# Kernel optimization log

Measured on AMD Instinct MI355X. Metric: run time of the kernel, lower is better.

## Reference

```python
import jax, jax.numpy as jnp
import numpy as np

N0, N1, N2 = 100000, 20000, 4000
DEG = 10
G_NODES = 200000
D, ED, CD, FF, NHEAD = 512, 256, 300, 2048, 2


def _layernorm(x, g, b, eps=1e-5):
    m = jnp.mean(x, -1, keepdims=True)
    v = jnp.var(x, -1, keepdims=True)
    return (x - m) * jax.lax.rsqrt(v + eps) * g + b


def _mha(q_in, kv_in, w_in, b_in, w_out, b_out):
    # torch nn.MultiheadAttention, inputs are (seq, batch, d)
    d = q_in.shape[-1]
    wq, wk, wv = w_in[:d], w_in[d:2 * d], w_in[2 * d:]
    bq, bk, bv = b_in[:d], b_in[d:2 * d], b_in[2 * d:]
    dh = d // NHEAD
    q = (q_in @ wq.T + bq).reshape(q_in.shape[0], q_in.shape[1], NHEAD, dh)
    k = (kv_in @ wk.T + bk).reshape(kv_in.shape[0], kv_in.shape[1], NHEAD, dh)
    v = (kv_in @ wv.T + bv).reshape(kv_in.shape[0], kv_in.shape[1], NHEAD, dh)
    scores = jnp.einsum('qnhd,knhd->nhqk', q, k) * (dh ** -0.5)
    o = jnp.einsum('nhqk,knhd->qnhd', jax.nn.softmax(scores, -1), v)
    o = o.reshape(q_in.shape[0], q_in.shape[1], d)
    return o @ w_out.T + b_out


def setup_inputs() -> dict:
    key = jax.random.key(0)
    k = lambda i: jax.random.fold_in(key, i)
    inp = {}
    inp['nid0'] = jax.random.randint(k(0), (N0,), 0, G_NODES, dtype=jnp.int32)
    inp['nid1'] = jax.random.randint(k(1), (N1,), 0, G_NODES, dtype=jnp.int32)
    inp['nid2'] = jax.random.randint(k(2), (N2,), 0, G_NODES, dtype=jnp.int32)
    inp['esrc0'] = jax.random.randint(k(3), (N1 * DEG,), 0, N0, dtype=jnp.int32)
    inp['edst0'] = jnp.repeat(jnp.arange(N1, dtype=jnp.int32), DEG)
    inp['esrc1'] = jax.random.randint(k(4), (N2 * DEG,), 0, N1, dtype=jnp.int32)
    inp['edst1'] = jnp.repeat(jnp.arange(N2, dtype=jnp.int32), DEG)
    inp['content0'] = jax.random.normal(k(5), (N0, CD), jnp.float32)
    inp['content1'] = jax.random.normal(k(6), (N1, CD), jnp.float32)
    inp['content2'] = jax.random.normal(k(7), (N2, CD), jnp.float32)
    inp['node_emb_w'] = jax.random.normal(k(8), (G_NODES + 1, ED), jnp.float32) / ED
    inp['ee_w'] = jax.random.normal(k(9), (D, ED), jnp.float32) * 0.06
    inp['ee_b'] = jax.random.normal(k(10), (D,), jnp.float32) * 0.001
    inp['proj_w'] = jax.random.normal(k(11), (D, CD), jnp.float32) * 0.06
    inp['proj_b'] = jax.random.normal(k(12), (D,), jnp.float32) * 0.001
    inp['proj_g'] = jnp.ones((D,), jnp.float32)
    inp['proj_beta'] = jnp.zeros((D,), jnp.float32)
    L = 2  # decoder layers
    inp['sa_in_w'] = jax.random.normal(k(13), (L, 3 * D, D), jnp.float32) * 0.04
    inp['sa_in_b'] = jnp.zeros((L, 3 * D), jnp.float32)
    inp['sa_out_w'] = jax.random.normal(k(14), (L, D, D), jnp.float32) * 0.04
    inp['sa_out_b'] = jnp.zeros((L, D), jnp.float32)
    inp['ca_in_w'] = jax.random.normal(k(15), (L, 3 * D, D), jnp.float32) * 0.04
    inp['ca_in_b'] = jnp.zeros((L, 3 * D), jnp.float32)
    inp['ca_out_w'] = jax.random.normal(k(16), (L, D, D), jnp.float32) * 0.04
    inp['ca_out_b'] = jnp.zeros((L, D), jnp.float32)
    inp['lin1_w'] = jax.random.normal(k(17), (L, FF, D), jnp.float32) * 0.03
    inp['lin1_b'] = jnp.zeros((L, FF), jnp.float32)
    inp['lin2_w'] = jax.random.normal(k(18), (L, D, FF), jnp.float32) * 0.03
    inp['lin2_b'] = jnp.zeros((L, D), jnp.float32)
    for n in ('n1', 'n2', 'n3'):
        inp[n + '_g'] = jnp.ones((L, D), jnp.float32)
        inp[n + '_b'] = jnp.zeros((L, D), jnp.float32)
    return inp


def _forward(nid0, nid1, nid2, esrc0, edst0, esrc1, edst1,
             content0, content1, content2, node_emb_w, ee_w, ee_b,
             proj_w, proj_b, proj_g, proj_beta,
             sa_in_w, sa_in_b, sa_out_w, sa_out_b,
             ca_in_w, ca_in_b, ca_out_w, ca_out_b,
             lin1_w, lin1_b, lin2_w, lin2_b,
             n1_g, n1_b, n2_g, n2_b, n3_g, n3_b):
    def node_h(nid, content):
        nh = node_emb_w[nid + 1] @ ee_w.T + ee_b           # emb_expand(node_emb(nid+1))
        c = _layernorm(jax.nn.leaky_relu(content @ proj_w.T + proj_b, 0.1), proj_g, proj_beta)
        h = nh + c                                          # mix_embeddings (c[:, :D] == c)
        return h / jnp.maximum(jnp.linalg.norm(h, axis=1, keepdims=True), 1e-5)

    h0 = node_h(nid0, content0)
    h1 = node_h(nid1, content1)
    h2 = node_h(nid2, content2)

    def agg_mean(h_src, src, dst, n_dst):
        s = jax.ops.segment_sum(h_src[src], dst, num_segments=n_dst)
        w = jax.ops.segment_sum(jnp.ones(src.shape[0], h_src.dtype), dst, num_segments=n_dst)
        return s / w[:, None]

    # block 0: non-prediction GraphConv -> concat(mean_agg, h), L2 normalize
    m1 = agg_mean(h0, esrc0, edst0, N1)
    h1 = jnp.concatenate([m1, h1], axis=1)                  # (N1, 2D)
    h1 = h1 / jnp.maximum(jnp.linalg.norm(h1, axis=1, keepdims=True), 1e-5)

    # block 1: prediction GraphConv -> transformer-decoder fusion
    m2 = agg_mean(h1, esrc1, edst1, N2)                     # (N2, 2D)
    mem = m2.reshape(N2, 2, D).transpose(1, 0, 2)           # (n_layer=2, N2, D)
    tgt = h2[None]                                          # (1, N2, D)
    for l in range(2):  # post-norm TransformerDecoderLayer, gelu, dropout=0
        t2 = _mha(tgt, tgt, sa_in_w[l], sa_in_b[l], sa_out_w[l], sa_out_b[l])
        tgt = _layernorm(tgt + t2, n1_g[l], n1_b[l])
        t2 = _mha(tgt, mem, ca_in_w[l], ca_in_b[l], ca_out_w[l], ca_out_b[l])
        tgt = _layernorm(tgt + t2, n2_g[l], n2_b[l])
        ff = jax.nn.gelu(tgt @ lin1_w[l].T + lin1_b[l], approximate=False) @ lin2_w[l].T + lin2_b[l]
        tgt = _layernorm(tgt + ff, n3_g[l], n3_b[l])
    out = tgt[0]                                            # squeeze -> (N2, D)
    return out / jnp.maximum(jnp.linalg.norm(out, axis=1, keepdims=True), 1e-5)


def reference(nid0, nid1, nid2, esrc0, edst0, esrc1, edst1,
              content0, content1, content2, node_emb_w, ee_w, ee_b,
              proj_w, proj_b, proj_g, proj_beta,
              sa_in_w, sa_in_b, sa_out_w, sa_out_b,
              ca_in_w, ca_in_b, ca_out_w, ca_out_b,
              lin1_w, lin1_b, lin2_w, lin2_b,
              n1_g, n1_b, n2_g, n2_b, n3_g, n3_b):
    return _forward(nid0, nid1, nid2, esrc0, edst0, esrc1, edst1,
                    content0, content1, content2, node_emb_w, ee_w, ee_b,
                    proj_w, proj_b, proj_g, proj_beta,
                    sa_in_w, sa_in_b, sa_out_w, sa_out_b,
                    ca_in_w, ca_in_b, ca_out_w, ca_out_b,
                    lin1_w, lin1_b, lin2_w, lin2_b,
                    n1_g, n1_b, n2_g, n2_b, n3_g, n3_b)
```

## Files before the change

kernel.cpp:

```cpp
#include <hip/hip_runtime.h>
#include <math.h>

static constexpr int kN0  = 100000;
static constexpr int kN1  = 20000;
static constexpr int kN2  = 4000;
static constexpr int kDeg = 10;
static constexpr int kD   = 512;
static constexpr int kFF  = 2048;
static constexpr int kRows  = 48;
static constexpr int kRowsN = 32;
static constexpr int kLdA  = 584;
static constexpr int kLdG  = 520;

using short8  = __attribute__((ext_vector_type(8))) short;
using floatx4 = __attribute__((ext_vector_type(4))) float;

__device__ inline unsigned short f2bf(float f) {
    union { float f; unsigned u; } v; v.f = f;
    unsigned r = v.u + 0x7FFFu + ((v.u >> 16) & 1u);
    return (unsigned short)(r >> 16);
}

__global__ __launch_bounds__(256) void pack_node_w_kernel(
    const float* __restrict__ ee_w, const float* __restrict__ proj_w,
    ushort* __restrict__ Bp)
{
    int tid  = blockIdx.x * 256 + threadIdx.x;
    int lane = tid & 63;
    int tile = tid >> 6;
    int n     = (tile & 31) * 16 + (lane & 15);
    int kbase = (tile >> 5) * 32 + (lane >> 4) * 8;
    ushort v[8];
    #pragma unroll
    for (int j = 0; j < 8; ++j) {
        int k = kbase + j;
        float f = 0.f;
        if (k < 256)      f = ee_w[(size_t)n * 256 + k];
        else if (k < 556) f = proj_w[(size_t)n * 300 + (k - 256)];
        v[j] = f2bf(f);
    }
    uint4 u;
    u.x = (unsigned)v[0] | ((unsigned)v[1] << 16);
    u.y = (unsigned)v[2] | ((unsigned)v[3] << 16);
    u.z = (unsigned)v[4] | ((unsigned)v[5] << 16);
    u.w = (unsigned)v[6] | ((unsigned)v[7] << 16);
    *(uint4*)(Bp + (size_t)tid * 8) = u;
}

__global__ __launch_bounds__(256) void pack512_many_kernel(
    const float* __restrict__ sa_in_w, const float* __restrict__ sa_out_w,
    const float* __restrict__ ca_in_w, const float* __restrict__ ca_out_w,
    ushort* __restrict__ dst)
{
    int y = blockIdx.y, l = y / 6, m = y % 6;
    const float* W;
    switch (m) {
        case 0: W = sa_in_w  + (size_t)l * 3 * kD * kD + (size_t)2 * kD * kD; break;
        case 1: W = sa_out_w + (size_t)l * kD * kD; break;
        case 2: W = ca_in_w  + (size_t)l * 3 * kD * kD; break;
        case 3: W = ca_in_w  + (size_t)l * 3 * kD * kD + (size_t)kD * kD; break;
        case 4: W = ca_in_w  + (size_t)l * 3 * kD * kD + (size_t)2 * kD * kD; break;
        default:W = ca_out_w + (size_t)l * kD * kD; break;
    }
    int tid  = blockIdx.x * 256 + threadIdx.x;
    int lane = tid & 63;
    int tile = tid >> 6;
    int n  = (tile & 31) * 16 + (lane & 15);
    int kb = (tile >> 5) * 32 + (lane >> 4) * 8;
    const float* src = W + (size_t)n * 512 + kb;
    ushort v[8];
    #pragma unroll
    for (int j = 0; j < 8; ++j) v[j] = f2bf(src[j]);
    uint4 u;
    u.x = (unsigned)v[0] | ((unsigned)v[1] << 16);
    u.y = (unsigned)v[2] | ((unsigned)v[3] << 16);
    u.z = (unsigned)v[4] | ((unsigned)v[5] << 16);
    u.w = (unsigned)v[6] | ((unsigned)v[7] << 16);
    *(uint4*)(dst + (size_t)y * 262144 + (size_t)tid * 8) = u;
}

__global__ __launch_bounds__(256) void pack_generic_kernel(
    const float* __restrict__ src, size_t srcStride,
    ushort* __restrict__ dst, size_t dstStride, int N, int K)
{
    int tid  = blockIdx.x * 256 + threadIdx.x;
    int NT = N >> 4;
    int lane = tid & 63;
    int tile = tid >> 6;
    int ct = tile % NT, kc = tile / NT;
    int n  = ct * 16 + (lane & 15);
    int kb = kc * 32 + (lane >> 4) * 8;
    const float* W = src + blockIdx.y * srcStride + (size_t)n * K + kb;
    ushort v[8];
    #pragma unroll
    for (int j = 0; j < 8; ++j) v[j] = f2bf(W[j]);
    uint4 u;
    u.x = (unsigned)v[0] | ((unsigned)v[1] << 16);
    u.y = (unsigned)v[2] | ((unsigned)v[3] << 16);
    u.z = (unsigned)v[4] | ((unsigned)v[5] << 16);
    u.w = (unsigned)v[6] | ((unsigned)v[7] << 16);
    *(uint4*)(dst + blockIdx.y * dstStride + (size_t)tid * 8) = u;
}

__global__ __launch_bounds__(512, 4) void node_h_mfma(
    const int* __restrict__ nid,
    const float* __restrict__ content,
    const float* __restrict__ node_emb_w,
    const ushort* __restrict__ Bp,
    const float* __restrict__ ee_b, const float* __restrict__ proj_b,
    const float* __restrict__ proj_g, const float* __restrict__ proj_beta,
    float* __restrict__ hout, int ldh, int n)
{
    __shared__ __align__(16) ushort As[kRowsN * kLdA];
    __shared__ float redS[8][kRowsN], redQ[8][kRowsN];
    __shared__ float meanv[kRowsN], rstdv[kRowsN], rowinv[kRowsN];

    const int t    = threadIdx.x;
    const int lane = t & 63;
    const int wv   = t >> 6;
    const int quad = lane >> 4;
    const int l15  = lane & 15;
    const int row0 = blockIdx.x * kRowsN;

    #pragma unroll
    for (int it = 0; it < 9; ++it) {
        int flat = it * 512 + t;
        int r  = flat / 144;
        int k4 = flat - r * 144;
        int row = row0 + r; if (row >= n) row = n - 1;
        float4 f = make_float4(0.f, 0.f, 0.f, 0.f);
        if (k4 < 64)
            f = *(const float4*)(node_emb_w + ((size_t)(nid[row] + 1)) * 256 + k4 * 4);
        else if (k4 < 139)
            f = *(const float4*)(content + (size_t)row * 300 + (k4 - 64) * 4);
        ushort4 o = make_ushort4(f2bf(f.x), f2bf(f.y), f2bf(f.z), f2bf(f.w));
        *(ushort4*)(As + (size_t)r * kLdA + k4 * 4) = o;
    }
    __syncthreads();

    floatx4 acc[2][4] = {};
    const short8* BpV = (const short8*)Bp;

    #pragma unroll
    for (int kc = 8; kc < 18; ++kc) {
        const short8* bp = BpV + (size_t)(kc * 32 + wv * 4) * 64 + lane;
        short8 b0 = bp[0], b1 = bp[64], b2 = bp[128], b3 = bp[192];
        short8 a[2];
        #pragma unroll
        for (int rt = 0; rt < 2; ++rt)
            a[rt] = *(const short8*)(As + (size_t)(rt * 16 + l15) * kLdA + kc * 32 + quad * 8);
        #pragma unroll
        for (int rt = 0; rt < 2; ++rt) {
            acc[rt][0] = __builtin_amdgcn_mfma_f32_16x16x32_bf16(a[rt], b0, acc[rt][0], 0, 0, 0);
            acc[rt][1] = __builtin_amdgcn_mfma_f32_16x16x32_bf16(a[rt], b1, acc[rt][1], 0, 0, 0);
            acc[rt][2] = __builtin_amdgcn_mfma_f32_16x16x32_bf16(a[rt], b2, acc[rt][2], 0, 0, 0);
            acc[rt][3] = __builtin_amdgcn_mfma_f32_16x16x32_bf16(a[rt], b3, acc[rt][3], 0, 0, 0);
        }
    }

    const int colbase = wv * 64 + l15;
    float pb[4], pg[4], pbt[4], eb[4];
    #pragma unroll
    for (int ct = 0; ct < 4; ++ct) {
        int c = colbase + ct * 16;
        pb[ct]  = proj_b[c];
        pg[ct]  = proj_g[c];
        pbt[ct] = proj_beta[c];
        eb[ct]  = ee_b[c];
    }

    float s8[8], q8[8];
    #pragma unroll
    for (int rt = 0; rt < 2; ++rt) {
        #pragma unroll
        for (int i = 0; i < 4; ++i) {
            float s = 0.f, q = 0.f;
            #pragma unroll
            for (int ct = 0; ct < 4; ++ct) {
                float c = acc[rt][ct][i] + pb[ct];
                c = (c >= 0.f) ? c : 0.1f * c;
                acc[rt][ct][i] = c;
                s += c; q = fmaf(c, c, q);
            }
            s8[rt * 4 + i] = s; q8[rt * 4 + i] = q;
        }
    }
    #pragma unroll
    for (int idx = 0; idx < 8; ++idx) {
        #pragma unroll
        for (int m = 1; m < 16; m <<= 1) {
            s8[idx] += __shfl_xor(s8[idx], m);
            q8[idx] += __shfl_xor(q8[idx], m);
        }
    }
    if (l15 == 0) {
        #pragma unroll
        for (int rt = 0; rt < 2; ++rt)
            #pragma unroll
            for (int i = 0; i < 4; ++i) {
                int rl = rt * 16 + quad * 4 + i;
                redS[wv][rl] = s8[rt * 4 + i];
                redQ[wv][rl] = q8[rt * 4 + i];
            }
    }
    __syncthreads();
    if (t < kRowsN) {
        float s = 0.f, q = 0.f;
        #pragma unroll
        for (int w = 0; w < 8; ++w) { s += redS[w][t]; q += redQ[w][t]; }
        float m   = s * (1.f / 512.f);
        float var = q * (1.f / 512.f) - m * m;
        meanv[t] = m;
        rstdv[t] = rsqrtf(var + 1e-5f);
    }
    __syncthreads();

    #pragma unroll
    for (int rt = 0; rt < 2; ++rt) {
        #pragma unroll
        for (int i = 0; i < 4; ++i) {
            int rl = rt * 16 + quad * 4 + i;
            float m = meanv[rl], rs = rstdv[rl];
            #pragma unroll
            for (int ct = 0; ct < 4; ++ct)
                acc[rt][ct][i] = (acc[rt][ct][i] - m) * rs * pg[ct] + pbt[ct] + eb[ct];
        }
    }

    #pragma unroll
    for (int kc = 0; kc < 8; ++kc) {
        const short8* bp = BpV + (size_t)(kc * 32 + wv * 4) * 64 + lane;
        short8 b0 = bp[0], b1 = bp[64], b2 = bp[128], b3 = bp[192];
        short8 a[2];
        #pragma unroll
        for (int rt = 0; rt < 2; ++rt)
            a[rt] = *(const short8*)(As + (size_t)(rt * 16 + l15) * kLdA + kc * 32 + quad * 8);
        #pragma unroll
        for (int rt = 0; rt < 2; ++rt) {
            acc[rt][0] = __builtin_amdgcn_mfma_f32_16x16x32_bf16(a[rt], b0, acc[rt][0], 0, 0, 0);
            acc[rt][1] = __builtin_amdgcn_mfma_f32_16x16x32_bf16(a[rt], b1, acc[rt][1], 0, 0, 0);
            acc[rt][2] = __builtin_amdgcn_mfma_f32_16x16x32_bf16(a[rt], b2, acc[rt][2], 0, 0, 0);
            acc[rt][3] = __builtin_amdgcn_mfma_f32_16x16x32_bf16(a[rt], b3, acc[rt][3], 0, 0, 0);
        }
    }

    #pragma unroll
    for (int rt = 0; rt < 2; ++rt) {
        #pragma unroll
        for (int i = 0; i < 4; ++i) {
            float psq = 0.f;
            #pragma unroll
            for (int ct = 0; ct < 4; ++ct)
                psq = fmaf(acc[rt][ct][i], acc[rt][ct][i], psq);
            q8[rt * 4 + i] = psq;
        }
    }
    #pragma unroll
    for (int idx = 0; idx < 8; ++idx)
        #pragma unroll
        for (int m = 1; m < 16; m <<= 1)
            q8[idx] += __shfl_xor(q8[idx], m);
    if (l15 == 0) {
        #pragma unroll
        for (int rt = 0; rt < 2; ++rt)
            #pragma unroll
            for (int i = 0; i < 4; ++i)
                redS[wv][rt * 16 + quad * 4 + i] = q8[rt * 4 + i];
    }
    __syncthreads();
    if (t < kRowsN) {
        float s = 0.f;
        #pragma unroll
        for (int w = 0; w < 8; ++w) s += redS[w][t];
        rowinv[t] = 1.f / fmaxf(sqrtf(s), 1e-5f);
    }
    __syncthreads();

    #pragma unroll
    for (int rt = 0; rt < 2; ++rt) {
        #pragma unroll
        for (int i = 0; i < 4; ++i) {
            int rl = rt * 16 + quad * 4 + i;
            int grow = row0 + rl;
            if (grow < n) {
                float inv = rowinv[rl];
                float* dst = hout + (size_t)grow * ldh + colbase;
                #pragma unroll
                for (int ct = 0; ct < 4; ++ct)
                    dst[ct * 16] = acc[rt][ct][i] * inv;
            }
        }
    }
}

__device__ inline float gelu_exact(float x) {
    return 0.5f * x * (1.f + erff(x * 0.70710678118654752f));
}

template<int EPI>
__global__ __launch_bounds__(512, 2) void gemm_mfma(
    const float* __restrict__ A, int lda,
    const ushort* __restrict__ Bp, const float* __restrict__ bias,
    float* __restrict__ C, int ldc,
    const float* __restrict__ resid,
    const float* __restrict__ lng, const float* __restrict__ lnb,
    int M, int K, int N)
{
    __shared__ __align__(16) ushort As[kRows * kLdG];
    __shared__ float redS[8][kRows], redQ[8][kRows];
    __shared__ float meanv[kRows], rstdv[kRows];

    const int t    = threadIdx.x;
    const int lane = t & 63;
    const int wv   = t >> 6;
    const int quad = lane >> 4;
    const int l15  = lane & 15;
    const int row0 = blockIdx.x * kRows;
    const int nb   = blockIdx.y;
    const int NT   = N >> 4;

    floatx4 acc[3][4] = {};
    const short8* BpV = (const short8*)Bp;

    for (int k0 = 0; k0 < K; k0 += 512) {
        #pragma unroll
        for (int it = 0; it < 12; ++it) {
            int flat = it * 512 + t;
            int r  = flat >> 7;
            int k4 = flat & 127;
            int row = row0 + r; if (row >= M) row = M - 1;
            float4 f = *(const float4*)(A + (size_t)row * lda + k0 + k4 * 4);
            ushort4 o = make_ushort4(f2bf(f.x), f2bf(f.y), f2bf(f.z), f2bf(f.w));
            *(ushort4*)(As + (size_t)r * kLdG + k4 * 4) = o;
        }
        __syncthreads();
        const int g0 = k0 >> 5;
        #pragma unroll
        for (int kc = 0; kc < 16; ++kc) {
            const short8* bp = BpV + ((size_t)(g0 + kc) * NT + nb * 32 + wv * 4) * 64 + lane;
            short8 b0 = bp[0], b1 = bp[64], b2 = bp[128], b3 = bp[192];
            short8 a[3];
            #pragma unroll
            for (int rt = 0; rt < 3; ++rt)
                a[rt] = *(const short8*)(As + (size_t)(rt * 16 + l15) * kLdG + kc * 32 + quad * 8);
            #pragma unroll
            for (int rt = 0; rt < 3; ++rt) {
                acc[rt][0] = __builtin_amdgcn_mfma_f32_16x16x32_bf16(a[rt], b0, acc[rt][0], 0, 0, 0);
                acc[rt][1] = __builtin_amdgcn_mfma_f32_16x16x32_bf16(a[rt], b1, acc[rt][1], 0, 0, 0);
                acc[rt][2] = __builtin_amdgcn_mfma_f32_16x16x32_bf16(a[rt], b2, acc[rt][2], 0, 0, 0);
                acc[rt][3] = __builtin_amdgcn_mfma_f32_16x16x32_bf16(a[rt], b3, acc[rt][3], 0, 0, 0);
            }
        }
        __syncthreads();
    }

    const int colloc = wv * 64 + l15;
    float b[4];
    #pragma unroll
    for (int ct = 0; ct < 4; ++ct) b[ct] = bias[nb * 512 + colloc + ct * 16];

    if constexpr (EPI == 0 || EPI == 1) {
        #pragma unroll
        for (int rt = 0; rt < 3; ++rt) {
            #pragma unroll
            for (int i = 0; i < 4; ++i) {
                int row = row0 + rt * 16 + quad * 4 + i;
                if (row < M) {
                    float* dst = C + (size_t)row * ldc + nb * 512 + colloc;
                    #pragma unroll
                    for (int ct = 0; ct < 4; ++ct) {
                        float v = acc[rt][ct][i] + b[ct];
                        if (EPI == 1) v = gelu_exact(v);
                        dst[ct * 16] = v;
                    }
                }
            }
        }
    } else {
        float lg[4], lb[4];
        #pragma unroll
        for (int ct = 0; ct < 4; ++ct) {
            lg[ct] = lng[colloc + ct * 16];
            lb[ct] = lnb[colloc + ct * 16];
        }
        float s12[12], q12[12];
        #pragma unroll
        for (int rt = 0; rt < 3; ++rt) {
            #pragma unroll
            for (int i = 0; i < 4; ++i) {
                int rl = rt * 16 + quad * 4 + i;
                int row = row0 + rl; if (row >= M) row = M - 1;
                const float* rr = resid + (size_t)row * 512 + colloc;
                float s = 0.f, q = 0.f;
                #pragma unroll
                for (int ct = 0; ct < 4; ++ct) {
                    float h = acc[rt][ct][i] + b[ct] + rr[ct * 16];
                    acc[rt][ct][i] = h;
                    s += h; q = fmaf(h, h, q);
                }
                s12[rt * 4 + i] = s; q12[rt * 4 + i] = q;
            }
        }
        #pragma unroll
        for (int idx = 0; idx < 12; ++idx) {
            #pragma unroll
            for (int m = 1; m < 16; m <<= 1) {
                s12[idx] += __shfl_xor(s12[idx], m);
                q12[idx] += __shfl_xor(q12[idx], m);
            }
        }
        if (l15 == 0) {
            #pragma unroll
            for (int rt = 0; rt < 3; ++rt)
                #pragma unroll
                for (int i = 0; i < 4; ++i) {
                    int rl = rt * 16 + quad * 4 + i;
                    redS[wv][rl] = s12[rt * 4 + i];
                    redQ[wv][rl] = q12[rt * 4 + i];
                }
        }
        __syncthreads();
        if (t < kRows) {
            float s = 0.f, q = 0.f;
            #pragma unroll
            for (int w = 0; w < 8; ++w) { s += redS[w][t]; q += redQ[w][t]; }
            float m   = s * (1.f / 512.f);
            float var = q * (1.f / 512.f) - m * m;
            meanv[t] = m;
            rstdv[t] = rsqrtf(var + 1e-5f);
        }
        __syncthreads();
        #pragma unroll
        for (int rt = 0; rt < 3; ++rt) {
            #pragma unroll
            for (int i = 0; i < 4; ++i) {
                int rl = rt * 16 + quad * 4 + i;
                int row = row0 + rl;
                if (row < M) {
                    float m = meanv[rl], rs = rstdv[rl];
                    float* dst = C + (size_t)row * 512 + colloc;
                    #pragma unroll
                    for (int ct = 0; ct < 4; ++ct)
                        dst[ct * 16] = (acc[rt][ct][i] - m) * rs * lg[ct] + lb[ct];
                }
            }
        }
    }
}

__global__ __launch_bounds__(512, 2) void gemm3_mfma(
    const float* __restrict__ A0, const ushort* __restrict__ B0,
    const float* __restrict__ b0p, float* __restrict__ C0, int M0,
    const float* __restrict__ A1, const ushort* __restrict__ B1,
    const float* __restrict__ b1p, float* __restrict__ C1, int M1,
    const float* __restrict__ A2, const ushort* __restrict__ B2,
    const float* __restrict__ b2p, float* __restrict__ C2, int M2)
{
    __shared__ __align__(16) ushort As[kRows * kLdG];

    const int t    = threadIdx.x;
    const int lane = t & 63;
    const int wv   = t >> 6;
    const int quad = lane >> 4;
    const int l15  = lane & 15;

    const int g0 = (M0 + kRows - 1) / kRows;
    const int g1 = (M1 + kRows - 1) / kRows;
    int bx = blockIdx.x;
    const float* A; const ushort* Bw; const float* bias; float* C; int M;
    if (bx < g0)           { A = A0; Bw = B0; bias = b0p; C = C0; M = M0; }
    else if (bx < g0 + g1) { bx -= g0; A = A1; Bw = B1; bias = b1p; C = C1; M = M1; }
    else                   { bx -= g0 + g1; A = A2; Bw = B2; bias = b2p; C = C2; M = M2; }
    const int row0 = bx * kRows;

    floatx4 acc[3][4] = {};
    const short8* BpV = (const short8*)Bw;

    #pragma unroll
    for (int it = 0; it < 12; ++it) {
        int flat = it * 512 + t;
        int r  = flat >> 7;
        int k4 = flat & 127;
        int row = row0 + r; if (row >= M) row = M - 1;
        float4 f = *(const float4*)(A + (size_t)row * 512 + k4 * 4);
        ushort4 o = make_ushort4(f2bf(f.x), f2bf(f.y), f2bf(f.z), f2bf(f.w));
        *(ushort4*)(As + (size_t)r * kLdG + k4 * 4) = o;
    }
    __syncthreads();
    #pragma unroll
    for (int kc = 0; kc < 16; ++kc) {
        const short8* bp = BpV + ((size_t)kc * 32 + wv * 4) * 64 + lane;
        short8 b0 = bp[0], b1 = bp[64], b2 = bp[128], b3 = bp[192];
        short8 a[3];
        #pragma unroll
        for (int rt = 0; rt < 3; ++rt)
            a[rt] = *(const short8*)(As + (size_t)(rt * 16 + l15) * kLdG + kc * 32 + quad * 8);
        #pragma unroll
        for (int rt = 0; rt < 3; ++rt) {
            acc[rt][0] = __builtin_amdgcn_mfma_f32_16x16x32_bf16(a[rt], b0, acc[rt][0], 0, 0, 0);
            acc[rt][1] = __builtin_amdgcn_mfma_f32_16x16x32_bf16(a[rt], b1, acc[rt][1], 0, 0, 0);
            acc[rt][2] = __builtin_amdgcn_mfma_f32_16x16x32_bf16(a[rt], b2, acc[rt][2], 0, 0, 0);
            acc[rt][3] = __builtin_amdgcn_mfma_f32_16x16x32_bf16(a[rt], b3, acc[rt][3], 0, 0, 0);
        }
    }

    const int colloc = wv * 64 + l15;
    float b[4];
    #pragma unroll
    for (int ct = 0; ct < 4; ++ct) b[ct] = bias[colloc + ct * 16];
    #pragma unroll
    for (int rt = 0; rt < 3; ++rt) {
        #pragma unroll
        for (int i = 0; i < 4; ++i) {
            int row = row0 + rt * 16 + quad * 4 + i;
            if (row < M) {
                float* dst = C + (size_t)row * 512 + colloc;
                #pragma unroll
                for (int ct = 0; ct < 4; ++ct)
                    dst[ct * 16] = acc[rt][ct][i] + b[ct];
            }
        }
    }
}

__device__ inline float block_sum256(float v, float* red4) {
    #pragma unroll
    for (int off = 32; off > 0; off >>= 1) v += __shfl_down(v, off);
    if ((threadIdx.x & 63) == 0) red4[threadIdx.x >> 6] = v;
    __syncthreads();
    return red4[0] + red4[1] + red4[2] + red4[3];
}

__global__ __launch_bounds__(256) void agg_norm1_kernel(
    const float* __restrict__ h0, const int* __restrict__ esrc,
    float* __restrict__ h1cat)
{
    __shared__ int idx[kDeg];
    __shared__ float red4[4];
    int i = blockIdx.x, t = threadIdx.x;
    if (t < kDeg) idx[t] = esrc[i * kDeg + t];
    __syncthreads();
    float s0 = 0.f, s1 = 0.f;
    for (int e = 0; e < kDeg; ++e) {
        const float* hr = h0 + (size_t)idx[e] * 512;
        s0 += hr[t]; s1 += hr[t + 256];
    }
    s0 *= 0.1f; s1 *= 0.1f;
    size_t base = (size_t)i * 1024;
    float o0 = h1cat[base + 512 + t];
    float o1 = h1cat[base + 768 + t];
    float tot = block_sum256(s0 * s0 + s1 * s1 + o0 * o0 + o1 * o1, red4);
    float inv = 1.f / fmaxf(sqrtf(tot), 1e-5f);
    h1cat[base + t]       = s0 * inv;
    h1cat[base + 256 + t] = s1 * inv;
    h1cat[base + 512 + t] = o0 * inv;
    h1cat[base + 768 + t] = o1 * inv;
}

__global__ __launch_bounds__(256) void agg2_kernel(
    const float* __restrict__ h1cat, const int* __restrict__ esrc,
    float* __restrict__ m2)
{
    __shared__ int idx[kDeg];
    int i = blockIdx.x, t = threadIdx.x;
    if (t < kDeg) idx[t] = esrc[i * kDeg + t];
    __syncthreads();
    float s0 = 0.f, s1 = 0.f, s2 = 0.f, s3 = 0.f;
    for (int e = 0; e < kDeg; ++e) {
        const float* hr = h1cat + (size_t)idx[e] * 1024;
        s0 += hr[t]; s1 += hr[t + 256]; s2 += hr[t + 512]; s3 += hr[t + 768];
    }
    size_t base = (size_t)i * 1024;
    m2[base + t]       = s0 * 0.1f;
    m2[base + 256 + t] = s1 * 0.1f;
    m2[base + 512 + t] = s2 * 0.1f;
    m2[base + 768 + t] = s3 * 0.1f;
}

__global__ __launch_bounds__(256) void attn_combine_kernel(
    const float* __restrict__ Q,
    const float* __restrict__ Kb, const float* __restrict__ Vb,
    float* __restrict__ O)
{
    __shared__ float red[4][4];
    __shared__ float a[4];
    int i = blockIdx.x, t = threadIdx.x;
    size_t base  = (size_t)i * 512;
    size_t base0 = (size_t)(2 * i) * 512;
    size_t base1 = base0 + 512;
    float q0 = Q[base + t], q1 = Q[base + t + 256];
    float p00 = q0 * Kb[base0 + t];
    float p01 = q0 * Kb[base1 + t];
    float p10 = q1 * Kb[base0 + t + 256];
    float p11 = q1 * Kb[base1 + t + 256];
    #pragma unroll
    for (int off = 32; off > 0; off >>= 1) {
        p00 += __shfl_down(p00, off);
        p01 += __shfl_down(p01, off);
        p10 += __shfl_down(p10, off);
        p11 += __shfl_down(p11, off);
    }
    int w = t >> 6;
    if ((t & 63) == 0) { red[w][0] = p00; red[w][1] = p01; red[w][2] = p10; red[w][3] = p11; }
    __syncthreads();
    if (t == 0) {
        float s00 = (red[0][0] + red[1][0] + red[2][0] + red[3][0]) * 0.0625f;
        float s01 = (red[0][1] + red[1][1] + red[2][1] + red[3][1]) * 0.0625f;
        float s10 = (red[0][2] + red[1][2] + red[2][2] + red[3][2]) * 0.0625f;
        float s11 = (red[0][3] + red[1][3] + red[2][3] + red[3][3]) * 0.0625f;
        float m0 = fmaxf(s00, s01);
        float e0 = expf(s00 - m0), e1 = expf(s01 - m0);
        float d0 = e0 + e1;
        a[0] = e0 / d0; a[1] = e1 / d0;
        float m1 = fmaxf(s10, s11);
        float f0 = expf(s10 - m1), f1 = expf(s11 - m1);
        float d1 = f0 + f1;
        a[2] = f0 / d1; a[3] = f1 / d1;
    }
    __syncthreads();
    O[base + t]       = a[0] * Vb[base0 + t]       + a[1] * Vb[base1 + t];
    O[base + t + 256] = a[2] * Vb[base0 + t + 256] + a[3] * Vb[base1 + t + 256];
}

__global__ __launch_bounds__(256) void final_norm_kernel(
    const float* __restrict__ tgt, float* __restrict__ out)
{
    __shared__ float red4[4];
    int i = blockIdx.x, t = threadIdx.x;
    size_t base = (size_t)i * 512;
    float v0 = tgt[base + t], v1 = tgt[base + t + 256];
    float tot = block_sum256(v0 * v0 + v1 * v1, red4);
    float inv = 1.f / fmaxf(sqrtf(tot), 1e-5f);
    out[base + t]       = v0 * inv;
    out[base + t + 256] = v1 * inv;
}

extern "C" void kernel_launch(void* const* d_in, const int* in_sizes, int n_in,
                              void* d_out, int out_size, void* d_ws, size_t ws_size,
                              hipStream_t stream)
{
    (void)in_sizes; (void)n_in; (void)out_size; (void)ws_size;
    const int*   nid0       = (const int*)d_in[0];
    const int*   nid1       = (const int*)d_in[1];
    const int*   nid2       = (const int*)d_in[2];
    const int*   esrc0      = (const int*)d_in[3];
    const int*   esrc1      = (const int*)d_in[5];
    const float* content0   = (const float*)d_in[7];
    const float* content1   = (const float*)d_in[8];
    const float* content2   = (const float*)d_in[9];
    const float* node_emb_w = (const float*)d_in[10];
    const float* ee_w       = (const float*)d_in[11];
    const float* ee_b       = (const float*)d_in[12];
    const float* proj_w     = (const float*)d_in[13];
    const float* proj_b     = (const float*)d_in[14];
    const float* proj_g     = (const float*)d_in[15];
    const float* proj_beta  = (const float*)d_in[16];
    const float* sa_in_w    = (const float*)d_in[17];
    const float* sa_in_b    = (const float*)d_in[18];
    const float* sa_out_w   = (const float*)d_in[19];
    const float* sa_out_b   = (const float*)d_in[20];
    const float* ca_in_w    = (const float*)d_in[21];
    const float* ca_in_b    = (const float*)d_in[22];
    const float* ca_out_w   = (const float*)d_in[23];
    const float* ca_out_b   = (const float*)d_in[24];
    const float* lin1_w     = (const float*)d_in[25];
    const float* lin1_b     = (const float*)d_in[26];
    const float* lin2_w     = (const float*)d_in[27];
    const float* lin2_b     = (const float*)d_in[28];
    const float* n1_g       = (const float*)d_in[29];
    const float* n1_b       = (const float*)d_in[30];
    const float* n2_g       = (const float*)d_in[31];
    const float* n2_b       = (const float*)d_in[32];
    const float* n3_g       = (const float*)d_in[33];
    const float* n3_b       = (const float*)d_in[34];

    float* ws = (float*)d_ws;
    size_t off = 0;
    float* h0    = ws + off; off += (size_t)kN0 * 512;
    float* h1cat = ws + off; off += (size_t)kN1 * 1024;
    float* m2    = ws + off; off += (size_t)kN2 * 1024;
    float* tgt   = ws + off; off += (size_t)kN2 * 512;
    float* Qb    = ws + off; off += (size_t)kN2 * 512;
    float* Kb    = ws + off; off += (size_t)2 * kN2 * 512;
    float* Vb    = ws + off; off += (size_t)2 * kN2 * 512;
    float* Ob    = ws + off; off += (size_t)kN2 * 512;
    float* ffh   = ws + off; off += (size_t)kN2 * 2048;
    ushort* BpNode = (ushort*)(ws + off); off += 147456;
    ushort* Pw512  = (ushort*)(ws + off); off += 12 * 262144 / 2;
    ushort* Pl1    = (ushort*)(ws + off); off += 2 * 1048576 / 2;
    ushort* Pl2    = (ushort*)(ws + off); off += 2 * 1048576 / 2;

    dim3 blk(256);

    pack_node_w_kernel<<<dim3(144), blk, 0, stream>>>(ee_w, proj_w, BpNode);
    pack512_many_kernel<<<dim3(128, 12), blk, 0, stream>>>(
        sa_in_w, sa_out_w, ca_in_w, ca_out_w, Pw512);
    pack_generic_kernel<<<dim3(512, 2), blk, 0, stream>>>(
        lin1_w, (size_t)kFF * kD, Pl1, 1048576, kFF, kD);
    pack_generic_kernel<<<dim3(512, 2), blk, 0, stream>>>(
        lin2_w, (size_t)kD * kFF, Pl2, 1048576, kD, kFF);

    node_h_mfma<<<dim3((kN0 + kRowsN - 1) / kRowsN), dim3(512), 0, stream>>>(
        nid0, content0, node_emb_w, BpNode, ee_b, proj_b, proj_g, proj_beta,
        h0, 512, kN0);
    node_h_mfma<<<dim3((kN1 + kRowsN - 1) / kRowsN), dim3(512), 0, stream>>>(
        nid1, content1, node_emb_w, BpNode, ee_b, proj_b, proj_g, proj_beta,
        h1cat + 512, 1024, kN1);
    node_h_mfma<<<dim3((kN2 + kRowsN - 1) / kRowsN), dim3(512), 0, stream>>>(
        nid2, content2, node_emb_w, BpNode, ee_b, proj_b, proj_g, proj_beta,
        tgt, 512, kN2);

    agg_norm1_kernel<<<dim3(kN1), blk, 0, stream>>>(h0, esrc0, h1cat);
    agg2_kernel<<<dim3(kN2), blk, 0, stream>>>(h1cat, esrc1, m2);

    const int M   = kN2;
    const int gM  = (M + kRows - 1) / kRows;
    const int gM2 = (2 * M + kRows - 1) / kRows;
    dim3 blk512(512);
    for (int l = 0; l < 2; ++l) {
        const ushort* sa_v_p   = Pw512 + (size_t)(l * 6 + 0) * 262144;
        const ushort* sa_out_p = Pw512 + (size_t)(l * 6 + 1) * 262144;
        const ushort* ca_q_p   = Pw512 + (size_t)(l * 6 + 2) * 262144;
        const ushort* ca_k_p   = Pw512 + (size_t)(l * 6 + 3) * 262144;
        const ushort* ca_v_p   = Pw512 + (size_t)(l * 6 + 4) * 262144;
        const ushort* ca_out_p = Pw512 + (size_t)(l * 6 + 5) * 262144;
        const ushort* l1_p     = Pl1 + (size_t)l * 1048576;
        const ushort* l2_p     = Pl2 + (size_t)l * 1048576;
        const float* sa_b = sa_in_b + (size_t)l * 3 * kD;
        const float* saob = sa_out_b + (size_t)l * kD;
        const float* ca_b = ca_in_b + (size_t)l * 3 * kD;
        const float* caob = ca_out_b + (size_t)l * kD;
        const float* l1b = lin1_b + (size_t)l * kFF;
        const float* l2b = lin2_b + (size_t)l * kD;

        gemm3_mfma<<<dim3(gM + gM2 + gM2), blk512, 0, stream>>>(
            tgt, sa_v_p, sa_b + 2 * kD, Qb, M,
            m2,  ca_k_p, ca_b + kD,     Kb, 2 * M,
            m2,  ca_v_p, ca_b + 2 * kD, Vb, 2 * M);

        gemm_mfma<2><<<dim3(gM, 1), blk512, 0, stream>>>(
            Qb, 512, sa_out_p, saob, tgt, 512,
            tgt, n1_g + l * kD, n1_b + l * kD, M, 512, 512);

        gemm_mfma<0><<<dim3(gM, 1), blk512, 0, stream>>>(
            tgt, 512, ca_q_p, ca_b, Qb, 512,
            nullptr, nullptr, nullptr, M, 512, 512);
        attn_combine_kernel<<<dim3(M), blk, 0, stream>>>(Qb, Kb, Vb, Ob);
        gemm_mfma<2><<<dim3(gM, 1), blk512, 0, stream>>>(
            Ob, 512, ca_out_p, caob, tgt, 512,
            tgt, n2_g + l * kD, n2_b + l * kD, M, 512, 512);

        gemm_mfma<1><<<dim3(gM, 4), blk512, 0, stream>>>(
            tgt, 512, l1_p, l1b, ffh, 2048,
            nullptr, nullptr, nullptr, M, 512, 2048);
        gemm_mfma<2><<<dim3(gM, 1), blk512, 0, stream>>>(
            ffh, 2048, l2_p, l2b, tgt, 512,
            tgt, n3_g + l * kD, n3_b + l * kD, M, 2048, 512);
    }

    final_norm_kernel<<<dim3(kN2), blk, 0, stream>>>(tgt, (float*)d_out);
}
```

Baseline: 1.112 ms.

## Store intermediate activations in bf16 and merge node-embedding launches

All intermediate activation buffers (h0, h1cat, m2, Q/K/V/O, ffh, and a bf16 copy of tgt) are now stored as bf16 instead of fp32. GEMMs load them directly without converting, and the gather/aggregate kernels widen bf16 to fp32 on read. This halves the memory traffic of the gather-heavy aggregation and of the GEMM A-operand loads. The three node_h launches are also merged into one grid. Storing aggregates and normalized vectors in bf16 adds extra rounding error before accumulation.

```diff
diff --git a/kernel.cpp b/kernel.cpp
--- a/kernel.cpp
+++ b/kernel.cpp
@@ -20,6 +20,9 @@
     unsigned r = v.u + 0x7FFFu + ((v.u >> 16) & 1u);
     return (unsigned short)(r >> 16);
 }
+__device__ inline float bf2f(ushort u) {
+    union { unsigned v; float f; } x; x.v = (unsigned)u << 16; return x.f;
+}
 
 __global__ __launch_bounds__(256) void pack_node_w_kernel(
     const float* __restrict__ ee_w, const float* __restrict__ proj_w,
@@ -103,13 +106,16 @@
 }
 
 __global__ __launch_bounds__(512, 4) void node_h_mfma(
-    const int* __restrict__ nid,
-    const float* __restrict__ content,
+    const int* __restrict__ nid0a, const float* __restrict__ content0a,
+    ushort* __restrict__ outB0, int n0,
+    const int* __restrict__ nid1a, const float* __restrict__ content1a,
+    ushort* __restrict__ outB1, int n1,
+    const int* __restrict__ nid2a, const float* __restrict__ content2a,
+    ushort* __restrict__ outB2, float* __restrict__ outF2, int n2,
     const float* __restrict__ node_emb_w,
     const ushort* __restrict__ Bp,
     const float* __restrict__ ee_b, const float* __restrict__ proj_b,
-    const float* __restrict__ proj_g, const float* __restrict__ proj_beta,
-    float* __restrict__ hout, int ldh, int n)
+    const float* __restrict__ proj_g, const float* __restrict__ proj_beta)
 {
     __shared__ __align__(16) ushort As[kRowsN * kLdA];
     __shared__ float redS[8][kRowsN], redQ[8][kRowsN];
@@ -120,7 +126,16 @@
     const int wv   = t >> 6;
     const int quad = lane >> 4;
     const int l15  = lane & 15;
-    const int row0 = blockIdx.x * kRowsN;
+
+    const int g0 = (n0 + kRowsN - 1) / kRowsN;
+    const int g1 = (n1 + kRowsN - 1) / kRowsN;
+    int bx = blockIdx.x;
+    const int* nid; const float* content; ushort* outB; float* outF = nullptr;
+    int ldh, n;
+    if (bx < g0)           { nid = nid0a; content = content0a; outB = outB0; ldh = 512;  n = n0; }
+    else if (bx < g0 + g1) { bx -= g0; nid = nid1a; content = content1a; outB = outB1; ldh = 1024; n = n1; }
+    else                   { bx -= g0 + g1; nid = nid2a; content = content2a; outB = outB2; outF = outF2; ldh = 512; n = n2; }
+    const int row0 = bx * kRowsN;
 
     #pragma unroll
     for (int it = 0; it < 9; ++it) {
@@ -284,10 +299,13 @@
             int grow = row0 + rl;
             if (grow < n) {
                 float inv = rowinv[rl];
-                float* dst = hout + (size_t)grow * ldh + colbase;
+                ushort* dB = outB + (size_t)grow * ldh + colbase;
                 #pragma unroll
-                for (int ct = 0; ct < 4; ++ct)
-                    dst[ct * 16] = acc[rt][ct][i] * inv;
+                for (int ct = 0; ct < 4; ++ct) {
+                    float v = acc[rt][ct][i] * inv;
+                    dB[ct * 16] = f2bf(v);
+                    if (outF) outF[(size_t)grow * ldh + colbase + ct * 16] = v;
+                }
             }
         }
     }
@@ -299,9 +317,9 @@
 
 template<int EPI>
 __global__ __launch_bounds__(512, 2) void gemm_mfma(
-    const float* __restrict__ A, int lda,
+    const ushort* __restrict__ A, int lda,
     const ushort* __restrict__ Bp, const float* __restrict__ bias,
-    float* __restrict__ C, int ldc,
+    ushort* __restrict__ Cb, float* __restrict__ Cf, int ldc,
     const float* __restrict__ resid,
     const float* __restrict__ lng, const float* __restrict__ lnb,
     int M, int K, int N)
@@ -324,14 +342,13 @@
 
     for (int k0 = 0; k0 < K; k0 += 512) {
         #pragma unroll
-        for (int it = 0; it < 12; ++it) {
+        for (int it = 0; it < 6; ++it) {
             int flat = it * 512 + t;
-            int r  = flat >> 7;
-            int k4 = flat & 127;
+            int r  = flat >> 6;
+            int k8 = flat & 63;
             int row = row0 + r; if (row >= M) row = M - 1;
-            float4 f = *(const float4*)(A + (size_t)row * lda + k0 + k4 * 4);
-            ushort4 o = make_ushort4(f2bf(f.x), f2bf(f.y), f2bf(f.z), f2bf(f.w));
-            *(ushort4*)(As + (size_t)r * kLdG + k4 * 4) = o;
+            short8 v = *(const short8*)(A + (size_t)row * lda + k0 + k8 * 8);
+            *(short8*)(As + (size_t)r * kLdG + k8 * 8) = v;
         }
         __syncthreads();
         const int g0 = k0 >> 5;
@@ -366,12 +383,12 @@
             for (int i = 0; i < 4; ++i) {
                 int row = row0 + rt * 16 + quad * 4 + i;
                 if (row < M) {
-                    float* dst = C + (size_t)row * ldc + nb * 512 + colloc;
+                    ushort* dst = Cb + (size_t)row * ldc + nb * 512 + colloc;
                     #pragma unroll
                     for (int ct = 0; ct < 4; ++ct) {
                         float v = acc[rt][ct][i] + b[ct];
                         if (EPI == 1) v = gelu_exact(v);
-                        dst[ct * 16] = v;
+                        dst[ct * 16] = f2bf(v);
                     }
                 }
             }
@@ -438,10 +455,14 @@
                 int row = row0 + rl;
                 if (row < M) {
                     float m = meanv[rl], rs = rstdv[rl];
-                    float* dst = C + (size_t)row * 512 + colloc;
+                    float*  dF = Cf + (size_t)row * 512 + colloc;
+                    ushort* dB = Cb + (size_t)row * 512 + colloc;
                     #pragma unroll
-                    for (int ct = 0; ct < 4; ++ct)
-                        dst[ct * 16] = (acc[rt][ct][i] - m) * rs * lg[ct] + lb[ct];
+                    for (int ct = 0; ct < 4; ++ct) {
+                        float v = (acc[rt][ct][i] - m) * rs * lg[ct] + lb[ct];
+                        dF[ct * 16] = v;
+                        dB[ct * 16] = f2bf(v);
+                    }
                 }
             }
         }
@@ -449,12 +470,12 @@
 }
 
 __global__ __launch_bounds__(512, 2) void gemm3_mfma(
-    const float* __restrict__ A0, const ushort* __restrict__ B0,
-    const float* __restrict__ b0p, float* __restrict__ C0, int M0,
-    const float* __restrict__ A1, const ushort* __restrict__ B1,
-    const float* __restrict__ b1p, float* __restrict__ C1, int M1,
-    const float* __restrict__ A2, const ushort* __restrict__ B2,
-    const float* __restrict__ b2p, float* __restrict__ C2, int M2)
+    const ushort* __restrict__ A0, const ushort* __restrict__ B0,
+    const float* __restrict__ b0p, ushort* __restrict__ C0, int M0,
+    const ushort* __restrict__ A1, const ushort* __restrict__ B1,
+    const float* __restrict__ b1p, ushort* __restrict__ C1, int M1,
+    const ushort* __restrict__ A2, const ushort* __restrict__ B2,
+    const float* __restrict__ b2p, ushort* __restrict__ C2, int M2)
 {
     __shared__ __align__(16) ushort As[kRows * kLdG];
 
@@ -467,7 +488,7 @@
     const int g0 = (M0 + kRows - 1) / kRows;
     const int g1 = (M1 + kRows - 1) / kRows;
     int bx = blockIdx.x;
-    const float* A; const ushort* Bw; const float* bias; float* C; int M;
+    const ushort* A; const ushort* Bw; const float* bias; ushort* C; int M;
     if (bx < g0)           { A = A0; Bw = B0; bias = b0p; C = C0; M = M0; }
     else if (bx < g0 + g1) { bx -= g0; A = A1; Bw = B1; bias = b1p; C = C1; M = M1; }
     else                   { bx -= g0 + g1; A = A2; Bw = B2; bias = b2p; C = C2; M = M2; }
@@ -477,14 +498,13 @@
     const short8* BpV = (const short8*)Bw;
 
     #pragma unroll
-    for (int it = 0; it < 12; ++it) {
+    for (int it = 0; it < 6; ++it) {
         int flat = it * 512 + t;
-        int r  = flat >> 7;
-        int k4 = flat & 127;
+        int r  = flat >> 6;
+        int k8 = flat & 63;
         int row = row0 + r; if (row >= M) row = M - 1;
-        float4 f = *(const float4*)(A + (size_t)row * 512 + k4 * 4);
-        ushort4 o = make_ushort4(f2bf(f.x), f2bf(f.y), f2bf(f.z), f2bf(f.w));
-        *(ushort4*)(As + (size_t)r * kLdG + k4 * 4) = o;
+        short8 v = *(const short8*)(A + (size_t)row * 512 + k8 * 8);
+        *(short8*)(As + (size_t)r * kLdG + k8 * 8) = v;
     }
     __syncthreads();
     #pragma unroll
@@ -514,10 +534,10 @@
         for (int i = 0; i < 4; ++i) {
             int row = row0 + rt * 16 + quad * 4 + i;
             if (row < M) {
-                float* dst = C + (size_t)row * 512 + colloc;
+                ushort* dst = C + (size_t)row * 512 + colloc;
                 #pragma unroll
                 for (int ct = 0; ct < 4; ++ct)
-                    dst[ct * 16] = acc[rt][ct][i] + b[ct];
+                    dst[ct * 16] = f2bf(acc[rt][ct][i] + b[ct]);
             }
         }
     }
@@ -532,8 +552,8 @@
 }
 
 __global__ __launch_bounds__(256) void agg_norm1_kernel(
-    const float* __restrict__ h0, const int* __restrict__ esrc,
-    float* __restrict__ h1cat)
+    const ushort* __restrict__ h0, const int* __restrict__ esrc,
+    ushort* __restrict__ h1cat)
 {
     __shared__ int idx[kDeg];
     __shared__ float red4[4];
@@ -542,24 +562,24 @@
     __syncthreads();
     float s0 = 0.f, s1 = 0.f;
     for (int e = 0; e < kDeg; ++e) {
-        const float* hr = h0 + (size_t)idx[e] * 512;
-        s0 += hr[t]; s1 += hr[t + 256];
+        const ushort* hr = h0 + (size_t)idx[e] * 512;
+        s0 += bf2f(hr[t]); s1 += bf2f(hr[t + 256]);
     }
     s0 *= 0.1f; s1 *= 0.1f;
     size_t base = (size_t)i * 1024;
-    float o0 = h1cat[base + 512 + t];
-    float o1 = h1cat[base + 768 + t];
+    float o0 = bf2f(h1cat[base + 512 + t]);
+    float o1 = bf2f(h1cat[base + 768 + t]);
     float tot = block_sum256(s0 * s0 + s1 * s1 + o0 * o0 + o1 * o1, red4);
     float inv = 1.f / fmaxf(sqrtf(tot), 1e-5f);
-    h1cat[base + t]       = s0 * inv;
-    h1cat[base + 256 + t] = s1 * inv;
-    h1cat[base + 512 + t] = o0 * inv;
-    h1cat[base + 768 + t] = o1 * inv;
+    h1cat[base + t]       = f2bf(s0 * inv);
+    h1cat[base + 256 + t] = f2bf(s1 * inv);
+    h1cat[base + 512 + t] = f2bf(o0 * inv);
+    h1cat[base + 768 + t] = f2bf(o1 * inv);
 }
 
 __global__ __launch_bounds__(256) void agg2_kernel(
-    const float* __restrict__ h1cat, const int* __restrict__ esrc,
-    float* __restrict__ m2)
+    const ushort* __restrict__ h1cat, const int* __restrict__ esrc,
+    ushort* __restrict__ m2)
 {
     __shared__ int idx[kDeg];
     int i = blockIdx.x, t = threadIdx.x;
@@ -567,20 +587,21 @@
     __syncthreads();
     float s0 = 0.f, s1 = 0.f, s2 = 0.f, s3 = 0.f;
     for (int e = 0; e < kDeg; ++e) {
-        const float* hr = h1cat + (size_t)idx[e] * 1024;
-        s0 += hr[t]; s1 += hr[t + 256]; s2 += hr[t + 512]; s3 += hr[t + 768];
+        const ushort* hr = h1cat + (size_t)idx[e] * 1024;
+        s0 += bf2f(hr[t]);       s1 += bf2f(hr[t + 256]);
+        s2 += bf2f(hr[t + 512]); s3 += bf2f(hr[t + 768]);
     }
     size_t base = (size_t)i * 1024;
-    m2[base + t]       = s0 * 0.1f;
-    m2[base + 256 + t] = s1 * 0.1f;
-    m2[base + 512 + t] = s2 * 0.1f;
-    m2[base + 768 + t] = s3 * 0.1f;
+    m2[base + t]       = f2bf(s0 * 0.1f);
+    m2[base + 256 + t] = f2bf(s1 * 0.1f);
+    m2[base + 512 + t] = f2bf(s2 * 0.1f);
+    m2[base + 768 + t] = f2bf(s3 * 0.1f);
 }
 
 __global__ __launch_bounds__(256) void attn_combine_kernel(
-    const float* __restrict__ Q,
-    const float* __restrict__ Kb, const float* __restrict__ Vb,
-    float* __restrict__ O)
+    const ushort* __restrict__ Q,
+    const ushort* __restrict__ Kb, const ushort* __restrict__ Vb,
+    ushort* __restrict__ O)
 {
     __shared__ float red[4][4];
     __shared__ float a[4];
@@ -588,11 +609,11 @@
     size_t base  = (size_t)i * 512;
     size_t base0 = (size_t)(2 * i) * 512;
     size_t base1 = base0 + 512;
-    float q0 = Q[base + t], q1 = Q[base + t + 256];
-    float p00 = q0 * Kb[base0 + t];
-    float p01 = q0 * Kb[base1 + t];
-    float p10 = q1 * Kb[base0 + t + 256];
-    float p11 = q1 * Kb[base1 + t + 256];
+    float q0 = bf2f(Q[base + t]), q1 = bf2f(Q[base + t + 256]);
+    float p00 = q0 * bf2f(Kb[base0 + t]);
+    float p01 = q0 * bf2f(Kb[base1 + t]);
+    float p10 = q1 * bf2f(Kb[base0 + t + 256]);
+    float p11 = q1 * bf2f(Kb[base1 + t + 256]);
     #pragma unroll
     for (int off = 32; off > 0; off >>= 1) {
         p00 += __shfl_down(p00, off);
@@ -618,8 +639,8 @@
         a[2] = f0 / d1; a[3] = f1 / d1;
     }
     __syncthreads();
-    O[base + t]       = a[0] * Vb[base0 + t]       + a[1] * Vb[base1 + t];
-    O[base + t + 256] = a[2] * Vb[base0 + t + 256] + a[3] * Vb[base1 + t + 256];
+    O[base + t]       = f2bf(a[0] * bf2f(Vb[base0 + t])       + a[1] * bf2f(Vb[base1 + t]));
+    O[base + t + 256] = f2bf(a[2] * bf2f(Vb[base0 + t + 256]) + a[3] * bf2f(Vb[base1 + t + 256]));
 }
 
 __global__ __launch_bounds__(256) void final_norm_kernel(
@@ -676,15 +697,16 @@
 
     float* ws = (float*)d_ws;
     size_t off = 0;
-    float* h0    = ws + off; off += (size_t)kN0 * 512;
-    float* h1cat = ws + off; off += (size_t)kN1 * 1024;
-    float* m2    = ws + off; off += (size_t)kN2 * 1024;
-    float* tgt   = ws + off; off += (size_t)kN2 * 512;
-    float* Qb    = ws + off; off += (size_t)kN2 * 512;
-    float* Kb    = ws + off; off += (size_t)2 * kN2 * 512;
-    float* Vb    = ws + off; off += (size_t)2 * kN2 * 512;
-    float* Ob    = ws + off; off += (size_t)kN2 * 512;
-    float* ffh   = ws + off; off += (size_t)kN2 * 2048;
+    ushort* h0b    = (ushort*)(ws + off); off += (size_t)kN0 * 512 / 2;
+    ushort* h1catb = (ushort*)(ws + off); off += (size_t)kN1 * 1024 / 2;
+    ushort* m2b    = (ushort*)(ws + off); off += (size_t)kN2 * 1024 / 2;
+    float*  tgt    = ws + off;            off += (size_t)kN2 * 512;
+    ushort* tgtb   = (ushort*)(ws + off); off += (size_t)kN2 * 512 / 2;
+    ushort* Qbb    = (ushort*)(ws + off); off += (size_t)kN2 * 512 / 2;
+    ushort* Kbb    = (ushort*)(ws + off); off += (size_t)2 * kN2 * 512 / 2;
+    ushort* Vbb    = (ushort*)(ws + off); off += (size_t)2 * kN2 * 512 / 2;
+    ushort* Obb    = (ushort*)(ws + off); off += (size_t)kN2 * 512 / 2;
+    ushort* ffhb   = (ushort*)(ws + off); off += (size_t)kN2 * 2048 / 2;
     ushort* BpNode = (ushort*)(ws + off); off += 147456;
     ushort* Pw512  = (ushort*)(ws + off); off += 12 * 262144 / 2;
     ushort* Pl1    = (ushort*)(ws + off); off += 2 * 1048576 / 2;
@@ -700,18 +722,19 @@
     pack_generic_kernel<<<dim3(512, 2), blk, 0, stream>>>(
         lin2_w, (size_t)kD * kFF, Pl2, 1048576, kD, kFF);
 
-    node_h_mfma<<<dim3((kN0 + kRowsN - 1) / kRowsN), dim3(512), 0, stream>>>(
-        nid0, content0, node_emb_w, BpNode, ee_b, proj_b, proj_g, proj_beta,
-        h0, 512, kN0);
-    node_h_mfma<<<dim3((kN1 + kRowsN - 1) / kRowsN), dim3(512), 0, stream>>>(
-        nid1, content1, node_emb_w, BpNode, ee_b, proj_b, proj_g, proj_beta,
-        h1cat + 512, 1024, kN1);
-    node_h_mfma<<<dim3((kN2 + kRowsN - 1) / kRowsN), dim3(512), 0, stream>>>(
-        nid2, content2, node_emb_w, BpNode, ee_b, proj_b, proj_g, proj_beta,
-        tgt, 512, kN2);
-
-    agg_norm1_kernel<<<dim3(kN1), blk, 0, stream>>>(h0, esrc0, h1cat);
-    agg2_kernel<<<dim3(kN2), blk, 0, stream>>>(h1cat, esrc1, m2);
+    {
+        int g0 = (kN0 + kRowsN - 1) / kRowsN;
+        int g1 = (kN1 + kRowsN - 1) / kRowsN;
+        int g2 = (kN2 + kRowsN - 1) / kRowsN;
+        node_h_mfma<<<dim3(g0 + g1 + g2), dim3(512), 0, stream>>>(
+            nid0, content0, h0b, kN0,
+            nid1, content1, h1catb + 512, kN1,
+            nid2, content2, tgtb, tgt, kN2,
+            node_emb_w, BpNode, ee_b, proj_b, proj_g, proj_beta);
+    }
+
+    agg_norm1_kernel<<<dim3(kN1), blk, 0, stream>>>(h0b, esrc0, h1catb);
+    agg2_kernel<<<dim3(kN2), blk, 0, stream>>>(h1catb, esrc1, m2b);
 
     const int M   = kN2;
     const int gM  = (M + kRows - 1) / kRows;
@@ -734,27 +757,27 @@
         const float* l2b = lin2_b + (size_t)l * kD;
 
         gemm3_mfma<<<dim3(gM + gM2 + gM2), blk512, 0, stream>>>(
-            tgt, sa_v_p, sa_b + 2 * kD, Qb, M,
-            m2,  ca_k_p, ca_b + kD,     Kb, 2 * M,
-            m2,  ca_v_p, ca_b + 2 * kD, Vb, 2 * M);
+            tgtb, sa_v_p, sa_b + 2 * kD, Qbb, M,
+            m2b,  ca_k_p, ca_b + kD,     Kbb, 2 * M,
+            m2b,  ca_v_p, ca_b + 2 * kD, Vbb, 2 * M);
 
         gemm_mfma<2><<<dim3(gM, 1), blk512, 0, stream>>>(
-            Qb, 512, sa_out_p, saob, tgt, 512,
+            Qbb, 512, sa_out_p, saob, tgtb, tgt, 512,
             tgt, n1_g + l * kD, n1_b + l * kD, M, 512, 512);
 
         gemm_mfma<0><<<dim3(gM, 1), blk512, 0, stream>>>(
-            tgt, 512, ca_q_p, ca_b, Qb, 512,
+            tgtb, 512, ca_q_p, ca_b, Qbb, nullptr, 512,
             nullptr, nullptr, nullptr, M, 512, 512);
-        attn_combine_kernel<<<dim3(M), blk, 0, stream>>>(Qb, Kb, Vb, Ob);
+        attn_combine_kernel<<<dim3(M), blk, 0, stream>>>(Qbb, Kbb, Vbb, Obb);
         gemm_mfma<2><<<dim3(gM, 1), blk512, 0, stream>>>(
-            Ob, 512, ca_out_p, caob, tgt, 512,
+            Obb, 512, ca_out_p, caob, tgtb, tgt, 512,
             tgt, n2_g + l * kD, n2_b + l * kD, M, 512, 512);
 
         gemm_mfma<1><<<dim3(gM, 4), blk512, 0, stream>>>(
-            tgt, 512, l1_p, l1b, ffh, 2048,
+            tgtb, 512, l1_p, l1b, ffhb, nullptr, 2048,
             nullptr, nullptr, nullptr, M, 512, 2048);
         gemm_mfma<2><<<dim3(gM, 1), blk512, 0, stream>>>(
-            ffh, 2048, l2_p, l2b, tgt, 512,
+            ffhb, 2048, l2_p, l2b, tgtb, tgt, 512,
             tgt, n3_g + l * kD, n3_b + l * kD, M, 2048, 512);
     }
 
```

After: 961.0 us. 13.6% less time.
